# Performance work log

Measured on AMD Instinct MI355X. Metric: run time of the kernel, lower is better.

The kernel has to match this reference:

```python
import jax, jax.numpy as jnp
import numpy as np

N_EMBED = 2048
N_HEAD = 16
HEAD_DIM = N_EMBED // N_HEAD
LN_EPS = 1e-5


def setup_inputs() -> dict:
    key = jax.random.key(0)
    ks = jax.random.split(key, 12)
    B, S, D = 4, 2048, N_EMBED
    s = 0.02
    inp = {
        "x": jax.random.normal(ks[0], (B, S, D), jnp.float32),
        "ln1_w": jnp.ones((D,), jnp.float32),
        "ln1_b": jnp.zeros((D,), jnp.float32),
        "Wqkv": jax.random.normal(ks[1], (3 * D, D), jnp.float32) * s,
        "bqkv": jnp.zeros((3 * D,), jnp.float32),
        "Wo": jax.random.normal(ks[2], (D, D), jnp.float32) * s,
        "bo": jnp.zeros((D,), jnp.float32),
        "ln2_w": jnp.ones((D,), jnp.float32),
        "ln2_b": jnp.zeros((D,), jnp.float32),
        "W1": jax.random.normal(ks[3], (4 * D, D), jnp.float32) * s,
        "b1": jnp.zeros((4 * D,), jnp.float32),
        "W2": jax.random.normal(ks[4], (D, 4 * D), jnp.float32) * s,
        "b2": jnp.zeros((D,), jnp.float32),
        # ALiBi slopes: 2^(-8*(h+1)/n_head)
        "slopes": jnp.asarray(2.0 ** (-8.0 * (np.arange(1, N_HEAD + 1)) / N_HEAD), jnp.float32),
    }
    return inp


def layer_norm(x, w, b):
    mu = jnp.mean(x, axis=-1, keepdims=True)
    var = jnp.mean(jnp.square(x - mu), axis=-1, keepdims=True)
    return (x - mu) * jax.lax.rsqrt(var + LN_EPS) * w + b


def attention(h, Wqkv, bqkv, Wo, bo, slopes):
    B, S, D = h.shape
    qkv = jnp.einsum("bsd,ed->bse", h, Wqkv) + bqkv  # [B,S,3D]
    q, k, v = jnp.split(qkv, 3, axis=-1)
    q = q.reshape(B, S, N_HEAD, HEAD_DIM).transpose(0, 2, 1, 3)
    k = k.reshape(B, S, N_HEAD, HEAD_DIM).transpose(0, 2, 1, 3)
    v = v.reshape(B, S, N_HEAD, HEAD_DIM).transpose(0, 2, 1, 3)
    scores = jnp.einsum("bhqd,bhkd->bhqk", q, k) / jnp.sqrt(jnp.float32(HEAD_DIM))
    pos = jnp.arange(S)
    rel = pos[None, :] - pos[:, None]  # j - i, <= 0 on causal part
    alibi = slopes[:, None, None] * rel[None, :, :].astype(jnp.float32)  # [H,S,S]
    causal = rel <= 0
    scores = jnp.where(causal[None, None], scores + alibi[None], -jnp.inf)
    attn = jax.nn.softmax(scores, axis=-1)
    out = jnp.einsum("bhqk,bhkd->bhqd", attn, v)
    out = out.transpose(0, 2, 1, 3).reshape(B, S, D)
    return jnp.einsum("bsd,ed->bse", out, Wo) + bo


def reference(x, ln1_w, ln1_b, Wqkv, bqkv, Wo, bo, ln2_w, ln2_b, W1, b1, W2, b2, slopes):
    # Pre-LN block; dropout in eval mode (identity)
    x = x + attention(layer_norm(x, ln1_w, ln1_b), Wqkv, bqkv, Wo, bo, slopes)
    h = layer_norm(x, ln2_w, ln2_b)
    h = jax.nn.gelu(jnp.einsum("bsd,fd->bsf", h, W1) + b1, approximate=False)
    x = x + jnp.einsum("bsf,df->bsd", h, W2) + b2
    return x
```

## Files before the change

kernel.cpp:

```cpp
#include <hip/hip_runtime.h>

typedef unsigned short ushort_t;
typedef __attribute__((ext_vector_type(8))) short short8;
typedef __attribute__((ext_vector_type(4))) float floatx4;
typedef __attribute__((ext_vector_type(4))) unsigned short ush4;

#define MFMA16x16x32(a, b, c) __builtin_amdgcn_mfma_f32_16x16x32_bf16(a, b, c, 0, 0, 0)

__device__ __forceinline__ float bf2f(ushort_t h) {
    unsigned int u = ((unsigned int)h) << 16;
    return __builtin_bit_cast(float, u);
}
__device__ __forceinline__ ushort_t f2bf(float f) {
    unsigned int u = __builtin_bit_cast(unsigned int, f);
    u += 0x7fffu + ((u >> 16) & 1u);
    return (ushort_t)(u >> 16);
}
__device__ __forceinline__ void gload_lds16(const ushort_t* g, ushort_t* l) {
    __builtin_amdgcn_global_load_lds(
        (const __attribute__((address_space(1))) unsigned int*)g,
        (__attribute__((address_space(3))) unsigned int*)l, 16, 0, 0);
}

__global__ __launch_bounds__(256) void conv_bf16(const float* __restrict__ in,
                                                 ushort_t* __restrict__ out, int n8) {
    int i = blockIdx.x * 256 + threadIdx.x;
    const int stride = gridDim.x * 256;
    for (; i < n8; i += stride) {
        const float* p = in + (size_t)i * 8;
        floatx4 a0 = *(const floatx4*)p;
        floatx4 a1 = *(const floatx4*)(p + 4);
        short8 o;
        o[0] = (short)f2bf(a0[0]); o[1] = (short)f2bf(a0[1]);
        o[2] = (short)f2bf(a0[2]); o[3] = (short)f2bf(a0[3]);
        o[4] = (short)f2bf(a1[0]); o[5] = (short)f2bf(a1[1]);
        o[6] = (short)f2bf(a1[2]); o[7] = (short)f2bf(a1[3]);
        *(short8*)(out + (size_t)i * 8) = o;
    }
}

template <int INF32>
__global__ __launch_bounds__(256) void ln_kernel(const void* __restrict__ in,
                                                 const ushort_t* __restrict__ w,
                                                 const ushort_t* __restrict__ b,
                                                 ushort_t* __restrict__ out) {
    const int row = blockIdx.x;
    const int tid = threadIdx.x;
    const size_t base = (size_t)row * 2048 + (size_t)tid * 8;
    float v[8];
    if (INF32) {
        const float* p = (const float*)in + base;
        floatx4 a0 = *(const floatx4*)p;
        floatx4 a1 = *(const floatx4*)(p + 4);
        v[0] = a0[0]; v[1] = a0[1]; v[2] = a0[2]; v[3] = a0[3];
        v[4] = a1[0]; v[5] = a1[1]; v[6] = a1[2]; v[7] = a1[3];
    } else {
        short8 hv = *(const short8*)((const ushort_t*)in + base);
        const ushort_t* hp = (const ushort_t*)&hv;
#pragma unroll
        for (int k = 0; k < 8; k++) v[k] = bf2f(hp[k]);
    }
    float s = 0.f, sq = 0.f;
#pragma unroll
    for (int k = 0; k < 8; k++) { s += v[k]; sq += v[k] * v[k]; }
#pragma unroll
    for (int m = 32; m; m >>= 1) { s += __shfl_xor(s, m); sq += __shfl_xor(sq, m); }
    __shared__ float red[8];
    const int wv = tid >> 6;
    if ((tid & 63) == 0) { red[wv] = s; red[4 + wv] = sq; }
    __syncthreads();
    s = red[0] + red[1] + red[2] + red[3];
    sq = red[4] + red[5] + red[6] + red[7];
    const float mu = s * (1.f / 2048.f);
    const float var = fmaxf(sq * (1.f / 2048.f) - mu * mu, 0.f);
    const float rs = rsqrtf(var + 1e-5f);
    short8 ov;
#pragma unroll
    for (int k = 0; k < 8; k++) {
        const int c = tid * 8 + k;
        float y = (v[k] - mu) * rs * bf2f(w[c]) + bf2f(b[c]);
        ov[k] = (short)f2bf(y);
    }
    *(short8*)(out + base) = ov;
}

template <int EPI>
__global__ __launch_bounds__(512, 2) void gemm256(const ushort_t* __restrict__ A,
                                                  const ushort_t* __restrict__ W,
                                                  const ushort_t* __restrict__ bias,
                                                  const void* __restrict__ res,
                                                  void* __restrict__ out,
                                                  int M, int N, int K) {
    __shared__ ushort_t smem[65536];
    const int tid = threadIdx.x;
    const int lane = tid & 63;
    const int wave = tid >> 6;
    const int la = lane & 15;
    const int qd = lane >> 4;
    const int wrow = (wave >> 2) * 128;
    const int wcol = (wave & 3) * 64;
    const int nbn = N >> 8;
    int bm, bn;
    {
        int wg = (int)blockIdx.x;
        const int cpx = (int)gridDim.x >> 3;
        wg = (wg & 7) * cpx + (wg >> 3);
        const int per = 8 * nbn;
        const int g = wg / per;
        const int rem = wg - g * per;
        bm = g * 8 + (rem & 7);
        bn = rem >> 3;
    }
    const int srow = tid >> 2;
    const int schunk = (tid & 3) ^ ((srow >> 1) & 3);
    const ushort_t* gA = A + (size_t)(bm * 256 + srow) * K + schunk * 8;
    const ushort_t* gB = W + (size_t)(bn * 256 + srow) * K + schunk * 8;
    const int wbase = (tid & ~63) * 8;
    const int kch = (qd ^ ((la >> 1) & 3)) * 8;

    floatx4 acc[8][4];
    const floatx4 z4 = {0.f, 0.f, 0.f, 0.f};
#pragma unroll
    for (int i = 0; i < 8; i++)
#pragma unroll
        for (int j = 0; j < 4; j++) acc[i][j] = z4;
    short8 a[4], b[4];

#define GBAR()                                    \
    do {                                          \
        asm volatile("" ::: "memory");            \
        __builtin_amdgcn_s_barrier();             \
        asm volatile("" ::: "memory");            \
    } while (0)
#define GLGKM0() asm volatile("s_waitcnt lgkmcnt(0)" ::: "memory")
#define GVM8() asm volatile("s_waitcnt vmcnt(8)" ::: "memory")
#define STGA(koff, b_)                                                                  \
    do {                                                                                \
        gload_lds16(gA + (size_t)(koff), smem + (b_)*16384 + wbase);                    \
        gload_lds16(gA + (size_t)128 * K + (size_t)(koff),                              \
                    smem + (b_)*16384 + 4096 + wbase);                                  \
    } while (0)
#define STGB(koff, b_)                                                                  \
    do {                                                                                \
        gload_lds16(gB + (size_t)(koff), smem + (b_)*16384 + 8192 + wbase);             \
        gload_lds16(gB + (size_t)128 * K + (size_t)(koff),                              \
                    smem + (b_)*16384 + 12288 + wbase);                                 \
    } while (0)
#define LDAF(b_, mh)                                                                    \
    do {                                                                                \
        _Pragma("unroll") for (int mi = 0; mi < 4; mi++) {                              \
            a[mi] = *(const short8*)&smem[(b_)*16384 +                                  \
                                          (wrow + (mh)*64 + mi * 16 + la) * 32 + kch];  \
        }                                                                               \
    } while (0)
#define LDBF(b_)                                                                        \
    do {                                                                                \
        _Pragma("unroll") for (int nj = 0; nj < 4; nj++) {                              \
            b[nj] = *(const short8*)&smem[(b_)*16384 + 8192 +                           \
                                          (wcol + nj * 16 + la) * 32 + kch];            \
        }                                                                               \
    } while (0)
#define MM16(mb)                                                                        \
    do {                                                                                \
        _Pragma("unroll") for (int mi = 0; mi < 4; mi++)                                \
            _Pragma("unroll") for (int nj = 0; nj < 4; nj++) acc[(mb) + mi][nj] =       \
                MFMA16x16x32(a[mi], b[nj], acc[(mb) + mi][nj]);                         \
    } while (0)
#define KITER(u)                                                                        \
    do {                                                                                \
        const int pre_ = (t + (u) + 3 < NT) ? (t + (u) + 3) : (NT - 1);                 \
        const size_t ko_ = (size_t)pre_ * 32;                                           \
        LDAF((u), 0); LDBF((u)); STGA(ko_, ((u) + 3) & 3);                              \
        GBAR(); GLGKM0();                                                               \
        __builtin_amdgcn_s_setprio(1); MM16(0); __builtin_amdgcn_s_setprio(0);          \
        GBAR();                                                                         \
        LDAF((u), 1); STGB(ko_, ((u) + 3) & 3);                                         \
        GBAR(); GLGKM0();                                                               \
        __builtin_amdgcn_s_setprio(1); MM16(4); __builtin_amdgcn_s_setprio(0);          \
        GVM8(); GBAR();                                                                 \
    } while (0)

    const int NT = K >> 5;
    STGA(0, 0); STGB(0, 0);
    STGA(32, 1); STGB(32, 1);
    STGA(64, 2); STGB(64, 2);
    GVM8(); GBAR();

    for (int t = 0; t < NT; t += 4) { KITER(0); KITER(1); KITER(2); KITER(3); }
    asm volatile("s_waitcnt vmcnt(0)" ::: "memory");
#undef GBAR
#undef GLGKM0
#undef GVM8
#undef STGA
#undef STGB
#undef LDAF
#undef LDBF
#undef MM16
#undef KITER

    if (EPI == 0) {
        ushort_t* q_out = (ushort_t*)out;
        if (bn < 16) {
            const float qs = (bn < 8) ? (0.08838834764831845f * 1.4426950408889634f) : 1.0f;
            ushort_t* dst = (bn < 8) ? q_out : (q_out + 16777216);
#pragma unroll
            for (int i = 0; i < 8; i++)
#pragma unroll
                for (int j = 0; j < 4; j++)
#pragma unroll
                    for (int r = 0; r < 4; r++) {
                        const int m = bm * 256 + wrow + i * 16 + qd * 4 + r;
                        const int n = bn * 256 + wcol + j * 16 + la;
                        dst[(size_t)m * 2048 + (n & 2047)] =
                            f2bf((acc[i][j][r] + bf2f(bias[n])) * qs);
                    }
        } else {
            ushort_t* v_out = q_out + 33554432;
#pragma unroll
            for (int i = 0; i < 8; i++)
#pragma unroll
                for (int j = 0; j < 4; j++) {
                    const int n = bn * 256 + wcol + j * 16 + la;
                    const int d = n - 4096;
                    const int m0 = bm * 256 + wrow + i * 16 + qd * 4;
                    const int bb = m0 >> 11, s = m0 & 2047;
                    const float bv = bf2f(bias[n]);
                    ush4 pk;
#pragma unroll
                    for (int r = 0; r < 4; r++) pk[r] = f2bf(acc[i][j][r] + bv);
                    *(ush4*)&v_out[((size_t)(bb * 2048 + d)) * 2048 + s] = pk;
                }
        }
    } else {
#pragma unroll
        for (int i = 0; i < 8; i++)
#pragma unroll
            for (int j = 0; j < 4; j++)
#pragma unroll
                for (int r = 0; r < 4; r++) {
                    const int m = bm * 256 + wrow + i * 16 + qd * 4 + r;
                    const int n = bn * 256 + wcol + j * 16 + la;
                    const size_t idx = (size_t)m * N + n;
                    float v = acc[i][j][r] + bf2f(bias[n]);
                    if (EPI == 1) {
                        v += ((const float*)res)[idx];
                        ((ushort_t*)out)[idx] = f2bf(v);
                    } else if (EPI == 2) {
                        v = 0.5f * v * (1.f + erff(v * 0.70710678118654752f));
                        ((ushort_t*)out)[idx] = f2bf(v);
                    } else {
                        v += bf2f(((const ushort_t*)res)[idx]);
                        ((float*)out)[idx] = v;
                    }
                }
    }
}

__global__ __launch_bounds__(256, 2) void attn_kernel(const ushort_t* __restrict__ qb,
                                                      const ushort_t* __restrict__ kb,
                                                      const ushort_t* __restrict__ vtb,
                                                      const float* __restrict__ slopes,
                                                      ushort_t* __restrict__ out) {
    __shared__ ushort_t Ks[16384];
    __shared__ ushort_t Vt[16384];
    __shared__ ushort_t Ps[4096];
    const int tid = threadIdx.x;
    const int lane = tid & 63;
    const int wave = tid >> 6;
    const int la = lane & 15;
    const int qd = lane >> 4;
    const int lid = (int)blockIdx.x;
    const int pair = (lid & 7) * 8 + (lid >> 8);
    const int h = pair & 15;
    const int b = pair >> 4;
    const int qt = 31 - ((lid >> 3) & 31);
    const float slope2 = slopes[h] * 1.4426950408889634f;

    const size_t qrow = (size_t)(b * 2048 + qt * 64 + wave * 16 + la);
    short8 qa[4];
#pragma unroll
    for (int ks = 0; ks < 4; ks++)
        qa[ks] = *(const short8*)&qb[qrow * 2048 + h * 128 + (ks * 4 + qd) * 8];

    const ushort_t* kbase = kb + ((size_t)b * 2048) * 2048 + h * 128;
    const ushort_t* vbase = vtb + ((size_t)(b * 2048 + h * 128)) * 2048;

    floatx4 accO[8];
    const floatx4 z4 = {0.f, 0.f, 0.f, 0.f};
#pragma unroll
    for (int dt = 0; dt < 8; dt++) accO[dt] = z4;
    float mst[4] = {-1e30f, -1e30f, -1e30f, -1e30f};
    float lst[4] = {0.f, 0.f, 0.f, 0.f};

#define AISSUE(kt_, buf_)                                                                   \
    do {                                                                                    \
        _Pragma("unroll") for (int p_ = 0; p_ < 4; p_++) {                                  \
            const int f_ = p_ * 256 + tid;                                                  \
            const int r_ = f_ >> 4;                                                         \
            const int cs_ = f_ & 15;                                                        \
            gload_lds16(kbase + (size_t)((kt_) * 64 + r_) * 2048 + (cs_ ^ (r_ & 15)) * 8,   \
                        Ks + (buf_) * 8192 + (size_t)(p_ * 256 + (tid & ~63)) * 8);         \
        }                                                                                   \
        _Pragma("unroll") for (int p_ = 0; p_ < 4; p_++) {                                  \
            const int f_ = p_ * 256 + tid;                                                  \
            const int d_ = f_ >> 3;                                                         \
            const int c_ = f_ & 7;                                                          \
            gload_lds16(vbase + (size_t)d_ * 2048 + (kt_) * 64 + (c_ ^ (d_ & 7)) * 8,       \
                        Vt + (buf_) * 8192 + (size_t)(p_ * 256 + (tid & ~63)) * 8);         \
        }                                                                                   \
    } while (0)
#define ABAR()                                    \
    do {                                          \
        asm volatile("" ::: "memory");            \
        __builtin_amdgcn_s_barrier();             \
        asm volatile("" ::: "memory");            \
    } while (0)

    AISSUE(0, 0);
    for (int kt = 0; kt <= qt; kt++) {
        const int cur = kt & 1;
        if (kt < qt) {
            AISSUE(kt + 1, cur ^ 1);
            asm volatile("s_waitcnt vmcnt(8)" ::: "memory");
        } else {
            asm volatile("s_waitcnt vmcnt(0)" ::: "memory");
        }
        ABAR();
        const ushort_t* Kc = Ks + cur * 8192;
        const ushort_t* Vc = Vt + cur * 8192;

        floatx4 sc[4];
#pragma unroll
        for (int nt = 0; nt < 4; nt++) sc[nt] = z4;
#pragma unroll
        for (int nt = 0; nt < 4; nt++) {
#pragma unroll
            for (int ks = 0; ks < 4; ks++) {
                short8 kf = *(const short8*)&Kc[(nt * 16 + la) * 128 + ((ks * 4 + qd) ^ la) * 8];
                sc[nt] = MFMA16x16x32(qa[ks], kf, sc[nt]);
            }
        }

        const int knb = kt * 64;
        const bool diag = (kt == qt);
        ushort_t* Pw = Ps + wave * 1024;
        float acol[4];
#pragma unroll
        for (int nt = 0; nt < 4; nt++)
            acol[nt] = slope2 * (float)(knb + nt * 16 + la);
#pragma unroll
        for (int r = 0; r < 4; r++) {
            float rmax = -1e30f;
#pragma unroll
            for (int nt = 0; nt < 4; nt++) {
                float sval = sc[nt][r] + acol[nt];
                if (diag && (nt * 16 + la > wave * 16 + qd * 4 + r)) sval = -1e30f;
                sc[nt][r] = sval;
                rmax = fmaxf(rmax, sval);
            }
            rmax = fmaxf(rmax, __shfl_xor(rmax, 1));
            rmax = fmaxf(rmax, __shfl_xor(rmax, 2));
            rmax = fmaxf(rmax, __shfl_xor(rmax, 4));
            rmax = fmaxf(rmax, __shfl_xor(rmax, 8));
            const float mnew = fmaxf(mst[r], rmax);
            const int row = qd * 4 + r;
            float rsum = 0.f;
#pragma unroll
            for (int nt = 0; nt < 4; nt++) {
                const float pv = __builtin_amdgcn_exp2f(sc[nt][r] - mnew);
                rsum += pv;
                const int col = nt * 16 + la;
                Pw[row * 64 + ((col >> 3) ^ (row & 7)) * 8 + (col & 7)] = f2bf(pv);
            }
            rsum += __shfl_xor(rsum, 1);
            rsum += __shfl_xor(rsum, 2);
            rsum += __shfl_xor(rsum, 4);
            rsum += __shfl_xor(rsum, 8);
            const float alpha = __builtin_amdgcn_exp2f(mst[r] - mnew);
            mst[r] = mnew;
            lst[r] = lst[r] * alpha + rsum;
#pragma unroll
            for (int dt = 0; dt < 8; dt++) accO[dt][r] *= alpha;
        }

#pragma unroll
        for (int k2 = 0; k2 < 2; k2++) {
            short8 pa = *(const short8*)&Pw[la * 64 + ((k2 * 4 + qd) ^ (la & 7)) * 8];
#pragma unroll
            for (int dt = 0; dt < 8; dt++) {
                const int d = dt * 16 + la;
                short8 vf = *(const short8*)&Vc[d * 64 + ((k2 * 4 + qd) ^ (d & 7)) * 8];
                accO[dt] = MFMA16x16x32(pa, vf, accO[dt]);
            }
        }
        ABAR();
    }
#undef AISSUE
#undef ABAR

    const size_t orow0 = (size_t)b * 2048 + qt * 64 + wave * 16 + qd * 4;
#pragma unroll
    for (int r = 0; r < 4; r++) {
        const float inv = 1.f / lst[r];
#pragma unroll
        for (int dt = 0; dt < 8; dt++)
            out[(orow0 + r) * 2048 + h * 128 + dt * 16 + la] = f2bf(accO[dt][r] * inv);
    }
}

extern "C" void kernel_launch(void* const* d_in, const int* in_sizes, int n_in,
                              void* d_out, int out_size, void* d_ws, size_t ws_size,
                              hipStream_t stream) {
    (void)in_sizes; (void)n_in; (void)out_size; (void)ws_size;
    const float* x      = (const float*)d_in[0];
    const float* ln1w   = (const float*)d_in[1];
    const float* ln1b   = (const float*)d_in[2];
    const float* Wqkv   = (const float*)d_in[3];
    const float* bqkv   = (const float*)d_in[4];
    const float* Wo     = (const float*)d_in[5];
    const float* bo     = (const float*)d_in[6];
    const float* ln2w   = (const float*)d_in[7];
    const float* ln2b   = (const float*)d_in[8];
    const float* W1     = (const float*)d_in[9];
    const float* b1     = (const float*)d_in[10];
    const float* W2     = (const float*)d_in[11];
    const float* b2     = (const float*)d_in[12];
    const float* slopes = (const float*)d_in[13];
    float* outp = (float*)d_out;

    char* ws = (char*)d_ws;
    const size_t MB = 1ull << 20;
    ushort_t* wbuf  = (ushort_t*)(ws);
    ushort_t* sv    = (ushort_t*)(ws + 36 * MB);
    ushort_t* ln1w_c = sv;
    ushort_t* ln1b_c = sv + 2048;
    ushort_t* bqkv_c = sv + 4096;
    ushort_t* bo_c   = sv + 10240;
    ushort_t* ln2w_c = sv + 12288;
    ushort_t* ln2b_c = sv + 14336;
    ushort_t* b1_c   = sv + 16384;
    ushort_t* b2_c   = sv + 24576;
    ushort_t* h_buf    = (ushort_t*)(ws + 37 * MB);
    ushort_t* q_buf    = (ushort_t*)(ws + 69 * MB);
    ushort_t* k_buf    = (ushort_t*)(ws + 101 * MB);
    ushort_t* vt_buf   = (ushort_t*)(ws + 133 * MB);
    ushort_t* attn_buf = (ushort_t*)(ws + 165 * MB);
    ushort_t* act_buf  = q_buf;
    ushort_t* x2_buf   = (ushort_t*)(ws + 197 * MB);

    const int M = 8192;

    conv_bf16<<<8, 256, 0, stream>>>(ln1w, ln1w_c, 2048 / 8);
    conv_bf16<<<8, 256, 0, stream>>>(ln1b, ln1b_c, 2048 / 8);
    ln_kernel<1><<<M, 256, 0, stream>>>(x, ln1w_c, ln1b_c, h_buf);
    conv_bf16<<<2048, 256, 0, stream>>>(Wqkv, wbuf, (6144 * 2048) / 8);
    conv_bf16<<<8, 256, 0, stream>>>(bqkv, bqkv_c, 6144 / 8);
    gemm256<0><<<(M / 256) * (6144 / 256), 512, 0, stream>>>(
        h_buf, wbuf, bqkv_c, nullptr, q_buf, M, 6144, 2048);
    attn_kernel<<<2048, 256, 0, stream>>>(q_buf, k_buf, vt_buf, slopes, attn_buf);
    conv_bf16<<<1024, 256, 0, stream>>>(Wo, wbuf, (2048 * 2048) / 8);
    conv_bf16<<<8, 256, 0, stream>>>(bo, bo_c, 2048 / 8);
    gemm256<1><<<(M / 256) * (2048 / 256), 512, 0, stream>>>(
        attn_buf, wbuf, bo_c, x, x2_buf, M, 2048, 2048);
    conv_bf16<<<8, 256, 0, stream>>>(ln2w, ln2w_c, 2048 / 8);
    conv_bf16<<<8, 256, 0, stream>>>(ln2b, ln2b_c, 2048 / 8);
    ln_kernel<0><<<M, 256, 0, stream>>>(x2_buf, ln2w_c, ln2b_c, h_buf);
    conv_bf16<<<2048, 256, 0, stream>>>(W1, wbuf, (8192 * 2048) / 8);
    conv_bf16<<<8, 256, 0, stream>>>(b1, b1_c, 8192 / 8);
    gemm256<2><<<(M / 256) * (8192 / 256), 512, 0, stream>>>(
        h_buf, wbuf, b1_c, nullptr, act_buf, M, 8192, 2048);
    conv_bf16<<<2048, 256, 0, stream>>>(W2, wbuf, (2048 * 8192) / 8);
    conv_bf16<<<8, 256, 0, stream>>>(b2, b2_c, 2048 / 8);
    gemm256<3><<<(M / 256) * (2048 / 256), 512, 0, stream>>>(
        act_buf, wbuf, b2_c, x2_buf, outp, M, 2048, 8192);
}
```

Baseline: 1.263 ms.

## Restructure GEMM to 4 waves with 128x128 per-wave tiles and triple buffering

The 256x256 GEMM now runs with 256 threads (4 waves) instead of 512 (8 waves). Each wave computes a 128x128 sub-tile with 8x8 MFMA accumulators, which raises the reuse of each LDS fragment load. The 4-stage LDS ring with split half-iterations becomes a 3-stage ring with one barrier pair per k-step, so LDS drops to 96KB. The cost is heavy register pressure (256 accumulator floats per lane) and only 4 waves per block to hide latency, with one block per CU.

```diff
diff --git a/kernel.cpp b/kernel.cpp
--- a/kernel.cpp
+++ b/kernel.cpp
@@ -85,20 +85,20 @@
 }
 
 template <int EPI>
-__global__ __launch_bounds__(512, 2) void gemm256(const ushort_t* __restrict__ A,
+__global__ __launch_bounds__(256, 1) void gemm256(const ushort_t* __restrict__ A,
                                                   const ushort_t* __restrict__ W,
                                                   const ushort_t* __restrict__ bias,
                                                   const void* __restrict__ res,
                                                   void* __restrict__ out,
                                                   int M, int N, int K) {
-    __shared__ ushort_t smem[65536];
+    __shared__ ushort_t smem[49152];
     const int tid = threadIdx.x;
     const int lane = tid & 63;
     const int wave = tid >> 6;
     const int la = lane & 15;
     const int qd = lane >> 4;
-    const int wrow = (wave >> 2) * 128;
-    const int wcol = (wave & 3) * 64;
+    const int wrow = (wave >> 1) * 128;
+    const int wcol = (wave & 1) * 128;
     const int nbn = N >> 8;
     int bm, bn;
     {
@@ -112,19 +112,19 @@
         bn = rem >> 3;
     }
     const int srow = tid >> 2;
-    const int schunk = (tid & 3) ^ ((srow >> 1) & 3);
+    const int schunk = (tid & 3) ^ ((tid >> 3) & 3);
     const ushort_t* gA = A + (size_t)(bm * 256 + srow) * K + schunk * 8;
     const ushort_t* gB = W + (size_t)(bn * 256 + srow) * K + schunk * 8;
-    const int wbase = (tid & ~63) * 8;
+    ushort_t* const lw = smem + (size_t)(tid & ~63) * 8;
     const int kch = (qd ^ ((la >> 1) & 3)) * 8;
 
-    floatx4 acc[8][4];
+    floatx4 acc[8][8];
     const floatx4 z4 = {0.f, 0.f, 0.f, 0.f};
 #pragma unroll
     for (int i = 0; i < 8; i++)
 #pragma unroll
-        for (int j = 0; j < 4; j++) acc[i][j] = z4;
-    short8 a[4], b[4];
+        for (int j = 0; j < 8; j++) acc[i][j] = z4;
+    short8 a[8], b[8];
 
 #define GBAR()                                    \
     do {                                          \
@@ -134,69 +134,57 @@
     } while (0)
 #define GLGKM0() asm volatile("s_waitcnt lgkmcnt(0)" ::: "memory")
 #define GVM8() asm volatile("s_waitcnt vmcnt(8)" ::: "memory")
-#define STGA(koff, b_)                                                                  \
+#define STG(kof, b_)                                                                    \
     do {                                                                                \
-        gload_lds16(gA + (size_t)(koff), smem + (b_)*16384 + wbase);                    \
-        gload_lds16(gA + (size_t)128 * K + (size_t)(koff),                              \
-                    smem + (b_)*16384 + 4096 + wbase);                                  \
-    } while (0)
-#define STGB(koff, b_)                                                                  \
+        _Pragma("unroll") for (int p_ = 0; p_ < 4; p_++)                                \
+            gload_lds16(gA + (size_t)(kof) + (size_t)p_ * 64 * K,                       \
+                        lw + (b_) * 16384 + p_ * 2048);                                 \
+        _Pragma("unroll") for (int p_ = 0; p_ < 4; p_++)                                \
+            gload_lds16(gB + (size_t)(kof) + (size_t)p_ * 64 * K,                       \
+                        lw + (b_) * 16384 + 8192 + p_ * 2048);                          \
+    } while (0)
+#define LDAF(b_)                                                                        \
     do {                                                                                \
-        gload_lds16(gB + (size_t)(koff), smem + (b_)*16384 + 8192 + wbase);             \
-        gload_lds16(gB + (size_t)128 * K + (size_t)(koff),                              \
-                    smem + (b_)*16384 + 12288 + wbase);                                 \
-    } while (0)
-#define LDAF(b_, mh)                                                                    \
-    do {                                                                                \
-        _Pragma("unroll") for (int mi = 0; mi < 4; mi++) {                              \
-            a[mi] = *(const short8*)&smem[(b_)*16384 +                                  \
-                                          (wrow + (mh)*64 + mi * 16 + la) * 32 + kch];  \
-        }                                                                               \
+        _Pragma("unroll") for (int mi = 0; mi < 8; mi++)                                \
+            a[mi] = *(const short8*)&smem[(b_) * 16384 +                                \
+                                          (wrow + mi * 16 + la) * 32 + kch];            \
     } while (0)
 #define LDBF(b_)                                                                        \
     do {                                                                                \
-        _Pragma("unroll") for (int nj = 0; nj < 4; nj++) {                              \
-            b[nj] = *(const short8*)&smem[(b_)*16384 + 8192 +                           \
+        _Pragma("unroll") for (int nj = 0; nj < 8; nj++)                                \
+            b[nj] = *(const short8*)&smem[(b_) * 16384 + 8192 +                         \
                                           (wcol + nj * 16 + la) * 32 + kch];            \
-        }                                                                               \
-    } while (0)
-#define MM16(mb)                                                                        \
+    } while (0)
+#define MM64()                                                                          \
     do {                                                                                \
-        _Pragma("unroll") for (int mi = 0; mi < 4; mi++)                                \
-            _Pragma("unroll") for (int nj = 0; nj < 4; nj++) acc[(mb) + mi][nj] =       \
-                MFMA16x16x32(a[mi], b[nj], acc[(mb) + mi][nj]);                         \
-    } while (0)
-#define KITER(u)                                                                        \
-    do {                                                                                \
-        const int pre_ = (t + (u) + 3 < NT) ? (t + (u) + 3) : (NT - 1);                 \
-        const size_t ko_ = (size_t)pre_ * 32;                                           \
-        LDAF((u), 0); LDBF((u)); STGA(ko_, ((u) + 3) & 3);                              \
-        GBAR(); GLGKM0();                                                               \
-        __builtin_amdgcn_s_setprio(1); MM16(0); __builtin_amdgcn_s_setprio(0);          \
-        GBAR();                                                                         \
-        LDAF((u), 1); STGB(ko_, ((u) + 3) & 3);                                         \
-        GBAR(); GLGKM0();                                                               \
-        __builtin_amdgcn_s_setprio(1); MM16(4); __builtin_amdgcn_s_setprio(0);          \
-        GVM8(); GBAR();                                                                 \
+        _Pragma("unroll") for (int mi = 0; mi < 8; mi++)                                \
+            _Pragma("unroll") for (int nj = 0; nj < 8; nj++) acc[mi][nj] =              \
+                MFMA16x16x32(a[mi], b[nj], acc[mi][nj]);                                \
     } while (0)
 
     const int NT = K >> 5;
-    STGA(0, 0); STGB(0, 0);
-    STGA(32, 1); STGB(32, 1);
-    STGA(64, 2); STGB(64, 2);
+    STG(0, 0); STG(32, 1);
     GVM8(); GBAR();
 
-    for (int t = 0; t < NT; t += 4) { KITER(0); KITER(1); KITER(2); KITER(3); }
+    int bc = 0, bs = 2;
+    for (int t = 0; t < NT; ++t) {
+        const int pre = (t + 2 < NT) ? (t + 2) : (NT - 1);
+        LDAF(bc); LDBF(bc);
+        STG((size_t)pre * 32, bs);
+        GBAR(); GLGKM0();
+        __builtin_amdgcn_s_setprio(1); MM64(); __builtin_amdgcn_s_setprio(0);
+        GVM8(); GBAR();
+        bc = (bc == 2) ? 0 : bc + 1;
+        bs = (bs == 2) ? 0 : bs + 1;
+    }
     asm volatile("s_waitcnt vmcnt(0)" ::: "memory");
 #undef GBAR
 #undef GLGKM0
 #undef GVM8
-#undef STGA
-#undef STGB
+#undef STG
 #undef LDAF
 #undef LDBF
-#undef MM16
-#undef KITER
+#undef MM64
 
     if (EPI == 0) {
         ushort_t* q_out = (ushort_t*)out;
@@ -206,7 +194,7 @@
 #pragma unroll
             for (int i = 0; i < 8; i++)
 #pragma unroll
-                for (int j = 0; j < 4; j++)
+                for (int j = 0; j < 8; j++)
 #pragma unroll
                     for (int r = 0; r < 4; r++) {
                         const int m = bm * 256 + wrow + i * 16 + qd * 4 + r;
@@ -219,7 +207,7 @@
 #pragma unroll
             for (int i = 0; i < 8; i++)
 #pragma unroll
-                for (int j = 0; j < 4; j++) {
+                for (int j = 0; j < 8; j++) {
                     const int n = bn * 256 + wcol + j * 16 + la;
                     const int d = n - 4096;
                     const int m0 = bm * 256 + wrow + i * 16 + qd * 4;
@@ -235,7 +223,7 @@
 #pragma unroll
         for (int i = 0; i < 8; i++)
 #pragma unroll
-            for (int j = 0; j < 4; j++)
+            for (int j = 0; j < 8; j++)
 #pragma unroll
                 for (int r = 0; r < 4; r++) {
                     const int m = bm * 256 + wrow + i * 16 + qd * 4 + r;
@@ -455,22 +443,22 @@
     ln_kernel<1><<<M, 256, 0, stream>>>(x, ln1w_c, ln1b_c, h_buf);
     conv_bf16<<<2048, 256, 0, stream>>>(Wqkv, wbuf, (6144 * 2048) / 8);
     conv_bf16<<<8, 256, 0, stream>>>(bqkv, bqkv_c, 6144 / 8);
-    gemm256<0><<<(M / 256) * (6144 / 256), 512, 0, stream>>>(
+    gemm256<0><<<(M / 256) * (6144 / 256), 256, 0, stream>>>(
         h_buf, wbuf, bqkv_c, nullptr, q_buf, M, 6144, 2048);
     attn_kernel<<<2048, 256, 0, stream>>>(q_buf, k_buf, vt_buf, slopes, attn_buf);
     conv_bf16<<<1024, 256, 0, stream>>>(Wo, wbuf, (2048 * 2048) / 8);
     conv_bf16<<<8, 256, 0, stream>>>(bo, bo_c, 2048 / 8);
-    gemm256<1><<<(M / 256) * (2048 / 256), 512, 0, stream>>>(
+    gemm256<1><<<(M / 256) * (2048 / 256), 256, 0, stream>>>(
         attn_buf, wbuf, bo_c, x, x2_buf, M, 2048, 2048);
     conv_bf16<<<8, 256, 0, stream>>>(ln2w, ln2w_c, 2048 / 8);
     conv_bf16<<<8, 256, 0, stream>>>(ln2b, ln2b_c, 2048 / 8);
     ln_kernel<0><<<M, 256, 0, stream>>>(x2_buf, ln2w_c, ln2b_c, h_buf);
     conv_bf16<<<2048, 256, 0, stream>>>(W1, wbuf, (8192 * 2048) / 8);
     conv_bf16<<<8, 256, 0, stream>>>(b1, b1_c, 8192 / 8);
-    gemm256<2><<<(M / 256) * (8192 / 256), 512, 0, stream>>>(
+    gemm256<2><<<(M / 256) * (8192 / 256), 256, 0, stream>>>(
         h_buf, wbuf, b1_c, nullptr, act_buf, M, 8192, 2048);
     conv_bf16<<<2048, 256, 0, stream>>>(W2, wbuf, (2048 * 8192) / 8);
     conv_bf16<<<8, 256, 0, stream>>>(b2, b2_c, 2048 / 8);
-    gemm256<3><<<(M / 256) * (2048 / 256), 512, 0, stream>>>(
+    gemm256<3><<<(M / 256) * (2048 / 256), 256, 0, stream>>>(
         act_buf, wbuf, b2_c, x2_buf, outp, M, 2048, 8192);
 }
```

New measurement: 1.568 ms. 24.2% more time.
